# Kernel optimization log

Hardware: AMD Instinct MI355X
Metric: run time of the kernel (lower is better)

Reference implementation:

```python
import jax, jax.numpy as jnp
import numpy as np

N_NODES = 50000
DEG = 32
N_EDGES = N_NODES * DEG
NODE_FT_DIM = 64  # hardcoded in original forward
ALPHA = 0.2


def setup_inputs() -> dict:
    key = jax.random.key(0)
    ks = jax.random.split(key, 8)
    node_fts = jax.random.normal(ks[0], (N_NODES, 256), dtype=jnp.float32)
    edge_fts = jax.random.normal(ks[1], (N_EDGES, 32), dtype=jnp.float32)
    # edges sorted by source, fixed degree -> matches original repeat_interleave semantics
    src = jnp.repeat(jnp.arange(N_NODES, dtype=jnp.int64), DEG)
    dst = jax.random.randint(ks[2], (N_EDGES,), 0, N_NODES, dtype=jnp.int64)
    edges = jnp.stack([src, dst], axis=1)
    W_node = jax.random.normal(ks[3], (256, 64), dtype=jnp.float32) * 0.06
    W_edge = jax.random.normal(ks[4], (32, 64), dtype=jnp.float32) * 0.14
    a_node = jax.random.normal(ks[5], (128, 1), dtype=jnp.float32) * 0.12
    a_edge = jax.random.normal(ks[6], (128, 1), dtype=jnp.float32) * 0.12
    return {"node_fts": node_fts, "edge_fts": edge_fts, "edges": edges,
            "W_node": W_node, "W_edge": W_edge, "a_node": a_node, "a_edge": a_edge}


def _leaky(x):
    return jnp.where(x >= 0, x, ALPHA * x)


def reference(node_fts, edge_fts, edges, W_node, W_edge, a_node, a_edge):
    n_nodes = node_fts.shape[0]
    src, dst = edges[:, 0], edges[:, 1]
    edge_fts_padded = jnp.pad(edge_fts, ((0, 0), (0, NODE_FT_DIM - edge_fts.shape[1])))

    h_v = node_fts @ W_node   # [N, 64]
    e_v = edge_fts @ W_edge   # [E, 64]

    # attention logits: [h_src || h_dst] @ a_node == h@a1 gathered + h@a2 gathered
    a_n1, a_n2 = a_node[:NODE_FT_DIM, 0], a_node[NODE_FT_DIM:, 0]
    a_e1, a_e2 = a_edge[:NODE_FT_DIM, 0], a_edge[NODE_FT_DIM:, 0]
    node_att = _leaky((h_v @ a_n1)[src] + (h_v @ a_n2)[dst])          # [E]
    # edge branch replaces slot 1 with padded edge features
    edge_att = _leaky((h_v @ a_e1)[src] + edge_fts_padded @ a_e2)      # [E]

    def seg_softmax(att):
        w = jnp.exp(jnp.clip(att, -2.0, 2.0))
        denom = jax.ops.segment_sum(w, src, num_segments=n_nodes)
        return w / denom[src]

    node_att_norm = seg_softmax(node_att)
    edge_att_norm = seg_softmax(edge_att)
    node_att_var = jnp.var(node_att_norm, ddof=1)
    edge_att_var = jnp.var(edge_att_norm, ddof=1)

    node_out = jax.ops.segment_sum(h_v[dst] * node_att_norm[:, None], src, num_segments=n_nodes)
    # original indexes e_v (per-edge rows) with node indices dst; in-range since E > N
    edge_out = jax.ops.segment_sum(e_v[dst] * edge_att_norm[:, None], src, num_segments=n_nodes)
    return node_out, edge_out, node_att_var, edge_att_var
```

## Files before the change

### kernel.cpp

```cpp
#include <hip/hip_runtime.h>
#include <hip/hip_fp16.h>

#define ALPHA 0.2f
static constexpr int NN = 50000;
static constexpr long NE = (long)NN * 32;

typedef float f4v __attribute__((ext_vector_type(4)));
typedef float f2v __attribute__((ext_vector_type(2)));

static constexpr long WS_HN1 = 0;
static constexpr long WS_HN2 = NN;
static constexpr long WS_HE1 = 2L * NN;
static constexpr long WS_ST  = 3L * NN;
static constexpr long WS_P   = 5L * NN;
static constexpr long WS_HEV = 250560;

__global__ __launch_bounds__(256) void k_hv(const float* __restrict__ A,
                                            const float* __restrict__ W,
                                            const float* __restrict__ a_node,
                                            const float* __restrict__ a_edge,
                                            __half* __restrict__ hev,
                                            float* __restrict__ hn1,
                                            float* __restrict__ hn2,
                                            float* __restrict__ he1) {
    __shared__ float As[16][68];
    __shared__ float Ws[16][68];
    const int t  = threadIdx.x;
    const int m0 = blockIdx.x * 64;
    const int tr = t >> 4, tc = t & 15;
    const int lr = t >> 2, seg = t & 3;
    const int wk = t >> 4, wc = t & 15;

    float acc[4][4] = {};
    for (int k0 = 0; k0 < 256; k0 += 16) {
        int row = m0 + lr;
        float4 av = make_float4(0.f, 0.f, 0.f, 0.f);
        if (row < NN)
            av = *reinterpret_cast<const float4*>(&A[(long)row * 256 + k0 + seg * 4]);
        As[seg*4+0][lr] = av.x; As[seg*4+1][lr] = av.y;
        As[seg*4+2][lr] = av.z; As[seg*4+3][lr] = av.w;
        *reinterpret_cast<float4*>(&Ws[wk][wc*4]) =
            *reinterpret_cast<const float4*>(&W[(k0 + wk) * 64 + wc * 4]);
        __syncthreads();
        #pragma unroll
        for (int kk = 0; kk < 16; ++kk) {
            float4 a4 = *reinterpret_cast<const float4*>(&As[kk][tr*4]);
            float4 b4 = *reinterpret_cast<const float4*>(&Ws[kk][tc*4]);
            acc[0][0] += a4.x*b4.x; acc[0][1] += a4.x*b4.y; acc[0][2] += a4.x*b4.z; acc[0][3] += a4.x*b4.w;
            acc[1][0] += a4.y*b4.x; acc[1][1] += a4.y*b4.y; acc[1][2] += a4.y*b4.z; acc[1][3] += a4.y*b4.w;
            acc[2][0] += a4.z*b4.x; acc[2][1] += a4.z*b4.y; acc[2][2] += a4.z*b4.z; acc[2][3] += a4.z*b4.w;
            acc[3][0] += a4.w*b4.x; acc[3][1] += a4.w*b4.y; acc[3][2] += a4.w*b4.z; acc[3][3] += a4.w*b4.w;
        }
        __syncthreads();
    }

    float an1[4], an2[4], ae1[4];
    #pragma unroll
    for (int j = 0; j < 4; ++j) {
        an1[j] = a_node[tc*4 + j];
        an2[j] = a_node[64 + tc*4 + j];
        ae1[j] = a_edge[tc*4 + j];
    }

    #pragma unroll
    for (int q = 0; q < 4; ++q) {
        float p1 = 0.f, p2 = 0.f, p3 = 0.f;
        #pragma unroll
        for (int j = 0; j < 4; ++j) {
            p1 += acc[q][j] * an1[j];
            p2 += acc[q][j] * an2[j];
            p3 += acc[q][j] * ae1[j];
        }
        #pragma unroll
        for (int m = 1; m <= 8; m <<= 1) {
            p1 += __shfl_xor(p1, m);
            p2 += __shfl_xor(p2, m);
            p3 += __shfl_xor(p3, m);
        }
        int row = m0 + tr * 4 + q;
        if (row < NN) {
            ushort4 hp;
            hp.x = __half_as_ushort(__float2half(acc[q][0]));
            hp.y = __half_as_ushort(__float2half(acc[q][1]));
            hp.z = __half_as_ushort(__float2half(acc[q][2]));
            hp.w = __half_as_ushort(__float2half(acc[q][3]));
            *reinterpret_cast<ushort4*>(&hev[(long)row * 128 + tc * 4]) = hp;
            if (tc == 0) { hn1[row] = p1; hn2[row] = p2; he1[row] = p3; }
        }
    }
}

__global__ __launch_bounds__(256) void k_ev(const float* __restrict__ ef,
                                            const float* __restrict__ We,
                                            __half* __restrict__ hev) {
    const int lane = threadIdx.x & 63, w = threadIdx.x >> 6;
    const int r = blockIdx.x * 4 + w;
    float acc = 0.f;
    #pragma unroll
    for (int k = 0; k < 32; ++k)
        acc += ef[(long)r * 32 + k] * We[k * 64 + lane];
    hev[(long)r * 128 + 64 + lane] = __float2half(acc);
}

__global__ __launch_bounds__(256) void k_edge(const float* __restrict__ ef,
                                              const int*   __restrict__ edges,
                                              const float* __restrict__ a_edge,
                                              const float* __restrict__ hn1,
                                              const float* __restrict__ hn2,
                                              const float* __restrict__ he1,
                                              const __half* __restrict__ hev,
                                              float* __restrict__ st,
                                              float* __restrict__ out) {
    const int t = threadIdx.x;
    const int w = t >> 6, l = t & 63;
    const int n = blockIdx.x * 4 + w;
    const int i = l >> 1, h = l & 1;
    const long ebase = (long)n * 32;

    const int d = __builtin_nontemporal_load(&edges[(ebase + i) * 2 + 1]);

    const f4v* efb = reinterpret_cast<const f4v*>(&ef[(ebase + i) * 32 + h * 16]);
    f4v v0 = __builtin_nontemporal_load(efb + 0);
    f4v v1 = __builtin_nontemporal_load(efb + 1);
    f4v v2 = __builtin_nontemporal_load(efb + 2);
    f4v v3 = __builtin_nontemporal_load(efb + 3);

    float dot;
    {
        const float* ae = &a_edge[64 + h * 16];
        float4 a0q = *reinterpret_cast<const float4*>(ae);
        float4 a1q = *reinterpret_cast<const float4*>(ae + 4);
        float4 a2q = *reinterpret_cast<const float4*>(ae + 8);
        float4 a3q = *reinterpret_cast<const float4*>(ae + 12);
        dot = v0.x*a0q.x + v0.y*a0q.y + v0.z*a0q.z + v0.w*a0q.w
            + v1.x*a1q.x + v1.y*a1q.y + v1.z*a1q.z + v1.w*a1q.w
            + v2.x*a2q.x + v2.y*a2q.y + v2.z*a2q.z + v2.w*a2q.w
            + v3.x*a3q.x + v3.y*a3q.y + v3.z*a3q.z + v3.w*a3q.w;
    }
    dot += __shfl_xor(dot, 1);

    float attn = hn1[n] + hn2[d];
    attn = attn >= 0.f ? attn : ALPHA * attn;
    float wn = __expf(fminf(fmaxf(attn, -2.f), 2.f));

    float atte = he1[n] + dot;
    atte = atte >= 0.f ? atte : ALPHA * atte;
    float we = __expf(fminf(fmaxf(atte, -2.f), 2.f));

    float dn = wn, de = we;
    #pragma unroll
    for (int m = 2; m <= 32; m <<= 1) { dn += __shfl_xor(dn, m); de += __shfl_xor(de, m); }
    float nn = wn / dn, ne = we / de;

    float sqn = nn * nn, sqe = ne * ne;
    #pragma unroll
    for (int m = 2; m <= 32; m <<= 1) { sqn += __shfl_xor(sqn, m); sqe += __shfl_xor(sqe, m); }
    if (l == 0) { st[n] = sqn; st[NN + n] = sqe; }

    __half2 wpk = __floats2half2_rn(nn, ne);
    unsigned int wbits = *reinterpret_cast<unsigned int*>(&wpk);

    int sd = d;
    unsigned int sw = wbits;
    #pragma unroll
    for (int k = 2; k <= 32; k <<= 1) {
        #pragma unroll
        for (int j = k >> 1; j >= 1; j >>= 1) {
            int pd = __shfl_xor(sd, j << 1);
            unsigned int pw = (unsigned int)__shfl_xor((int)sw, j << 1);
            const bool iLower   = (i & j) == 0;
            const bool up       = (i & k) == 0;
            const bool want_min = (iLower == up);
            const bool take     = want_min ? (pd < sd) : (pd > sd);
            if (take) { sd = pd; sw = pw; }
        }
    }

    const bool isE = l >= 32;
    float a0 = 0.f, a1 = 0.f;
    #pragma unroll
    for (int c = 0; c < 4; ++c) {
        __half2 h2[8];
        #pragma unroll
        for (int u = 0; u < 8; ++u) {
            int du = __builtin_amdgcn_readlane(sd, 2 * (c * 8 + u));
            h2[u] = *reinterpret_cast<const __half2*>(&hev[(long)du * 128 + l * 2]);
        }
        #pragma unroll
        for (int u = 0; u < 8; ++u) {
            unsigned int wv = (unsigned int)__builtin_amdgcn_readlane((int)sw, 2 * (c * 8 + u));
            __half2 wp = *reinterpret_cast<__half2*>(&wv);
            float wt = isE ? __high2float(wp) : __low2float(wp);
            float2 f = __half22float2(h2[u]);
            a0 = fmaf(wt, f.x, a0);
            a1 = fmaf(wt, f.y, a1);
        }
        __builtin_amdgcn_sched_barrier(0);
    }

    long off = isE ? ((long)NN * 64 + (long)n * 64 + (l - 32) * 2)
                   : ((long)n * 64 + l * 2);
    f2v o; o.x = a0; o.y = a1;
    __builtin_nontemporal_store(o, reinterpret_cast<f2v*>(&out[off]));
}

__global__ __launch_bounds__(256) void k_red1(const float* __restrict__ st,
                                              float* __restrict__ part) {
    const int t = threadIdx.x;
    const int n = blockIdx.x * 256 + t;
    float v0 = 0.f, v1 = 0.f;
    if (n < NN) { v0 = st[n]; v1 = st[NN + n]; }
    #pragma unroll
    for (int m = 1; m <= 32; m <<= 1) { v0 += __shfl_xor(v0, m); v1 += __shfl_xor(v1, m); }
    __shared__ float ls[4][2];
    const int wv = t >> 6;
    if ((t & 63) == 0) { ls[wv][0] = v0; ls[wv][1] = v1; }
    __syncthreads();
    if (t == 0) {
        part[(long)blockIdx.x * 2]     = ls[0][0] + ls[1][0] + ls[2][0] + ls[3][0];
        part[(long)blockIdx.x * 2 + 1] = ls[0][1] + ls[1][1] + ls[2][1] + ls[3][1];
    }
}

__global__ __launch_bounds__(64) void k_red2(const float* __restrict__ part,
                                             float* __restrict__ out) {
    const int t = threadIdx.x;
    double v0 = 0.0, v1 = 0.0;
    for (int b = t; b < 196; b += 64) {
        v0 += (double)part[b * 2];
        v1 += (double)part[b * 2 + 1];
    }
    #pragma unroll
    for (int m = 1; m <= 32; m <<= 1) { v0 += __shfl_xor(v0, m); v1 += __shfl_xor(v1, m); }
    if (t == 0) {
        const double M = (double)NE;
        const double corr = (double)NN * (double)NN / M;
        out[6400000] = (float)((v0 - corr) / (M - 1.0));
        out[6400001] = (float)((v1 - corr) / (M - 1.0));
    }
}

extern "C" void kernel_launch(void* const* d_in, const int* in_sizes, int n_in,
                              void* d_out, int out_size, void* d_ws, size_t ws_size,
                              hipStream_t stream) {
    const float* node_fts = (const float*)d_in[0];
    const float* edge_fts = (const float*)d_in[1];
    const int*   edges    = (const int*)  d_in[2];
    const float* W_node   = (const float*)d_in[3];
    const float* W_edge   = (const float*)d_in[4];
    const float* a_node   = (const float*)d_in[5];
    const float* a_edge   = (const float*)d_in[6];
    float* out = (float*)d_out;
    float* ws  = (float*)d_ws;

    float*  hn1 = ws + WS_HN1;
    float*  hn2 = ws + WS_HN2;
    float*  he1 = ws + WS_HE1;
    float*  st  = ws + WS_ST;
    float*  prt = ws + WS_P;
    __half* hev = (__half*)(ws + WS_HEV);

    k_hv  <<<(NN + 63) / 64, 256, 0, stream>>>(node_fts, W_node, a_node, a_edge,
                                               hev, hn1, hn2, he1);
    k_ev  <<<NN / 4, 256, 0, stream>>>(edge_fts, W_edge, hev);
    k_edge<<<NN / 4, 256, 0, stream>>>(edge_fts, edges, a_edge, hn1, hn2, he1,
                                       hev, st, out);
    k_red1<<<196, 256, 0, stream>>>(st, prt);
    k_red2<<<1, 64, 0, stream>>>(prt, out);
}
```

Measured before the change: 162.8 us.

## Compute node projection GEMM with fp16 MFMA instead of scalar FMA tiles

```diff
diff --git a/kernel.cpp b/kernel.cpp
--- a/kernel.cpp
+++ b/kernel.cpp
@@ -7,6 +7,8 @@
 
 typedef float f4v __attribute__((ext_vector_type(4)));
 typedef float f2v __attribute__((ext_vector_type(2)));
+typedef _Float16 h8 __attribute__((ext_vector_type(8)));
+typedef float f32x4 __attribute__((ext_vector_type(4)));
 
 static constexpr long WS_HN1 = 0;
 static constexpr long WS_HN2 = NN;
@@ -23,71 +25,67 @@
                                             float* __restrict__ hn1,
                                             float* __restrict__ hn2,
                                             float* __restrict__ he1) {
-    __shared__ float As[16][68];
-    __shared__ float Ws[16][68];
-    const int t  = threadIdx.x;
-    const int m0 = blockIdx.x * 64;
-    const int tr = t >> 4, tc = t & 15;
-    const int lr = t >> 2, seg = t & 3;
-    const int wk = t >> 4, wc = t & 15;
-
-    float acc[4][4] = {};
-    for (int k0 = 0; k0 < 256; k0 += 16) {
-        int row = m0 + lr;
-        float4 av = make_float4(0.f, 0.f, 0.f, 0.f);
-        if (row < NN)
-            av = *reinterpret_cast<const float4*>(&A[(long)row * 256 + k0 + seg * 4]);
-        As[seg*4+0][lr] = av.x; As[seg*4+1][lr] = av.y;
-        As[seg*4+2][lr] = av.z; As[seg*4+3][lr] = av.w;
-        *reinterpret_cast<float4*>(&Ws[wk][wc*4]) =
-            *reinterpret_cast<const float4*>(&W[(k0 + wk) * 64 + wc * 4]);
-        __syncthreads();
-        #pragma unroll
-        for (int kk = 0; kk < 16; ++kk) {
-            float4 a4 = *reinterpret_cast<const float4*>(&As[kk][tr*4]);
-            float4 b4 = *reinterpret_cast<const float4*>(&Ws[kk][tc*4]);
-            acc[0][0] += a4.x*b4.x; acc[0][1] += a4.x*b4.y; acc[0][2] += a4.x*b4.z; acc[0][3] += a4.x*b4.w;
-            acc[1][0] += a4.y*b4.x; acc[1][1] += a4.y*b4.y; acc[1][2] += a4.y*b4.z; acc[1][3] += a4.y*b4.w;
-            acc[2][0] += a4.z*b4.x; acc[2][1] += a4.z*b4.y; acc[2][2] += a4.z*b4.z; acc[2][3] += a4.z*b4.w;
-            acc[3][0] += a4.w*b4.x; acc[3][1] += a4.w*b4.y; acc[3][2] += a4.w*b4.z; acc[3][3] += a4.w*b4.w;
-        }
-        __syncthreads();
-    }
-
-    float an1[4], an2[4], ae1[4];
-    #pragma unroll
-    for (int j = 0; j < 4; ++j) {
-        an1[j] = a_node[tc*4 + j];
-        an2[j] = a_node[64 + tc*4 + j];
-        ae1[j] = a_edge[tc*4 + j];
-    }
-
-    #pragma unroll
-    for (int q = 0; q < 4; ++q) {
-        float p1 = 0.f, p2 = 0.f, p3 = 0.f;
-        #pragma unroll
-        for (int j = 0; j < 4; ++j) {
-            p1 += acc[q][j] * an1[j];
-            p2 += acc[q][j] * an2[j];
-            p3 += acc[q][j] * ae1[j];
-        }
-        #pragma unroll
-        for (int m = 1; m <= 8; m <<= 1) {
-            p1 += __shfl_xor(p1, m);
-            p2 += __shfl_xor(p2, m);
-            p3 += __shfl_xor(p3, m);
-        }
-        int row = m0 + tr * 4 + q;
-        if (row < NN) {
-            ushort4 hp;
-            hp.x = __half_as_ushort(__float2half(acc[q][0]));
-            hp.y = __half_as_ushort(__float2half(acc[q][1]));
-            hp.z = __half_as_ushort(__float2half(acc[q][2]));
-            hp.w = __half_as_ushort(__float2half(acc[q][3]));
-            *reinterpret_cast<ushort4*>(&hev[(long)row * 128 + tc * 4]) = hp;
-            if (tc == 0) { hn1[row] = p1; hn2[row] = p2; he1[row] = p3; }
-        }
-    }
+    __shared__ _Float16 Wt[64][264];
+    const int t = threadIdx.x;
+    const int w = t >> 6, l = t & 63;
+    const int lm = l & 15, lq = l >> 4;
+
+    {
+        const int n_ = t & 63, kq = t >> 6;
+        #pragma unroll 8
+        for (int j = 0; j < 64; ++j) {
+            int k = kq * 64 + j;
+            Wt[n_][k] = (_Float16)W[k * 64 + n_];
+        }
+    }
+    __syncthreads();
+
+    const int mbase = blockIdx.x * 64 + w * 16;
+    const int m = mbase + lm;
+    const int arow = m < NN ? m : NN - 1;
+
+    f32x4 acc[4] = {};
+    #pragma unroll
+    for (int s = 0; s < 8; ++s) {
+        const int k0 = s * 32 + lq * 8;
+        float4 q0 = *reinterpret_cast<const float4*>(&A[(long)arow * 256 + k0]);
+        float4 q1 = *reinterpret_cast<const float4*>(&A[(long)arow * 256 + k0 + 4]);
+        h8 nf;
+        nf[0] = (_Float16)q0.x; nf[1] = (_Float16)q0.y;
+        nf[2] = (_Float16)q0.z; nf[3] = (_Float16)q0.w;
+        nf[4] = (_Float16)q1.x; nf[5] = (_Float16)q1.y;
+        nf[6] = (_Float16)q1.z; nf[7] = (_Float16)q1.w;
+        #pragma unroll
+        for (int c = 0; c < 4; ++c) {
+            h8 wf = *reinterpret_cast<const h8*>(&Wt[c * 16 + lm][k0]);
+            acc[c] = __builtin_amdgcn_mfma_f32_16x16x32_f16(wf, nf, acc[c], 0, 0, 0);
+        }
+    }
+
+    float p1 = 0.f, p2 = 0.f, p3 = 0.f;
+    #pragma unroll
+    for (int c = 0; c < 4; ++c) {
+        const int n0 = c * 16 + lq * 4;
+        ushort4 hp;
+        hp.x = __half_as_ushort(__float2half(acc[c][0]));
+        hp.y = __half_as_ushort(__float2half(acc[c][1]));
+        hp.z = __half_as_ushort(__float2half(acc[c][2]));
+        hp.w = __half_as_ushort(__float2half(acc[c][3]));
+        if (m < NN)
+            *reinterpret_cast<ushort4*>(&hev[(long)m * 128 + n0]) = hp;
+        #pragma unroll
+        for (int r = 0; r < 4; ++r) {
+            const int n = n0 + r;
+            const float hv = acc[c][r];
+            p1 += hv * a_node[n];
+            p2 += hv * a_node[64 + n];
+            p3 += hv * a_edge[n];
+        }
+    }
+    p1 += __shfl_xor(p1, 16); p1 += __shfl_xor(p1, 32);
+    p2 += __shfl_xor(p2, 16); p2 += __shfl_xor(p2, 32);
+    p3 += __shfl_xor(p3, 16); p3 += __shfl_xor(p3, 32);
+    if (l < 16 && m < NN) { hn1[m] = p1; hn2[m] = p2; he1[m] = p3; }
 }
 
 __global__ __launch_bounds__(256) void k_ev(const float* __restrict__ ef,
```

After: 146.5 us, median of 2. 1.11x faster.
